# Kernel optimization log

Hardware: AMD Instinct MI355X
Metric: run time of the kernel (lower is better)

## Reference

```python
import jax, jax.numpy as jnp
import numpy as np

N_NODES = 50000
N_EDGES = 800000
IN_F, HID, HEADS, OUT_F = 64, 64, 4, 64
NEG_SLOPE = 0.2


def _gat_conv(x, ei, W, a_src, a_dst, b, H, C):
    """PyG-style GATConv (eval mode, add_self_loops=True, concat=True).
    x: [N, F_in], ei: [2, E], W: [F_in, H*C], a_src/a_dst: [H, C], b: [H*C].
    """
    N = x.shape[0]
    h = (x @ W).reshape(N, H, C)                      # [N,H,C]
    asrc = jnp.einsum('nhc,hc->nh', h, a_src)         # [N,H]
    adst = jnp.einsum('nhc,hc->nh', h, a_dst)         # [N,H]
    src, dst = ei[0], ei[1]
    logits = jax.nn.leaky_relu(asrc[src] + adst[dst], NEG_SLOPE)  # [E,H]
    m = jax.ops.segment_max(logits, dst, num_segments=N)
    m = jnp.where(jnp.isfinite(m), m, 0.0)
    ex = jnp.exp(logits - m[dst])
    denom = jax.ops.segment_sum(ex, dst, num_segments=N)
    alpha = ex / (denom[dst] + 1e-16)                 # [E,H]
    msg = h[src] * alpha[:, :, None]                  # [E,H,C]
    out = jax.ops.segment_sum(msg, dst, num_segments=N)  # [N,H,C]
    return out.reshape(N, H * C) + b


def _add_self_loops(ei, n):
    loops = jnp.arange(n, dtype=ei.dtype)
    return jnp.concatenate([ei, jnp.stack([loops, loops])], axis=1)


def setup_inputs() -> dict:
    key = jax.random.key(0)
    ks = jax.random.split(key, 16)
    x = jax.random.normal(ks[0], (N_NODES, IN_F), dtype=jnp.float32)
    edge_index = jax.random.randint(ks[1], (2, N_EDGES), 0, N_NODES, dtype=jnp.int32)
    s = 0.1
    d = {'x': x, 'edge_index': edge_index}
    # layer 0: IN_F -> HID, HEADS heads
    d['W0'] = jax.random.normal(ks[2], (IN_F, HEADS * HID), jnp.float32) * s
    d['a_src0'] = jax.random.normal(ks[3], (HEADS, HID), jnp.float32) * s
    d['a_dst0'] = jax.random.normal(ks[4], (HEADS, HID), jnp.float32) * s
    d['b0'] = jnp.zeros((HEADS * HID,), jnp.float32)
    # layer 1: HEADS*HID -> HID, HEADS heads
    d['W1'] = jax.random.normal(ks[5], (HEADS * HID, HEADS * HID), jnp.float32) * s
    d['a_src1'] = jax.random.normal(ks[6], (HEADS, HID), jnp.float32) * s
    d['a_dst1'] = jax.random.normal(ks[7], (HEADS, HID), jnp.float32) * s
    d['b1'] = jnp.zeros((HEADS * HID,), jnp.float32)
    # layer 2: HEADS*HID -> OUT_F, 1 head
    d['W2'] = jax.random.normal(ks[8], (HEADS * HID, OUT_F), jnp.float32) * s
    d['a_src2'] = jax.random.normal(ks[9], (1, OUT_F), jnp.float32) * s
    d['a_dst2'] = jax.random.normal(ks[10], (1, OUT_F), jnp.float32) * s
    d['b2'] = jnp.zeros((OUT_F,), jnp.float32)
    return d


def reference(x, edge_index, W0, a_src0, a_dst0, b0, W1, a_src1, a_dst1, b1, W2, a_src2, a_dst2, b2):
    ei = _add_self_loops(edge_index, x.shape[0])
    h = _gat_conv(x, ei, W0, a_src0, a_dst0, b0, HEADS, HID)
    h = jax.nn.elu(h)  # dropout identity in eval
    h = _gat_conv(h, ei, W1, a_src1, a_dst1, b1, HEADS, HID)
    h = jax.nn.elu(h)
    out = _gat_conv(h, ei, W2, a_src2, a_dst2, b2, 1, OUT_F)
    return out
```

## Files before the change

### kernel.cpp

```cpp
#include <hip/hip_runtime.h>
#include <hip/hip_fp16.h>
#include <math.h>

#define NODES 50000
#define EDGES 800000
#define NB_SCAN ((NODES + 1023) / 1024)

typedef __attribute__((ext_vector_type(8))) _Float16 f16x8;
typedef __attribute__((ext_vector_type(4))) _Float16 f16x4;
typedef __attribute__((ext_vector_type(4))) float f32x4;

__device__ __forceinline__ float lrelu02(float x){ return x > 0.f ? x : 0.2f * x; }

__device__ __forceinline__ f32x4 shflx4(f32x4 v, int m){
  f32x4 r;
  r[0] = __shfl_xor(v[0], m); r[1] = __shfl_xor(v[1], m);
  r[2] = __shfl_xor(v[2], m); r[3] = __shfl_xor(v[3], m);
  return r;
}


__global__ __launch_bounds__(256) void gat_hist(const int* __restrict__ ei, int* __restrict__ cnt){
  int e = blockIdx.x * 256 + threadIdx.x;
  if (e < EDGES) atomicAdd(&cnt[ei[EDGES + e]], 1);
}

__global__ __launch_bounds__(256) void gat_blocksum(const int* __restrict__ cnt, int* __restrict__ bsums){
  __shared__ int sd[256];
  int t = threadIdx.x, b = blockIdx.x;
  int base = b * 1024 + t * 4, s = 0;
  #pragma unroll
  for (int j = 0; j < 4; j++){ int i = base + j; if (i < NODES) s += cnt[i]; }
  sd[t] = s; __syncthreads();
  for (int o = 128; o > 0; o >>= 1){ if (t < o) sd[t] += sd[t + o]; __syncthreads(); }
  if (t == 0) bsums[b] = sd[0];
}

__global__ __launch_bounds__(256) void gat_rowptr(int* __restrict__ cnt, const int* __restrict__ bsums,
                                                  int* __restrict__ row_ptr){
  __shared__ int sd[256];
  int t = threadIdx.x, b = blockIdx.x;
  int base = b * 1024 + t * 4;
  int c[4]; int s = 0;
  #pragma unroll
  for (int j = 0; j < 4; j++){
    int i = base + j;
    c[j] = (i < NODES) ? cnt[i] : 0;
    s += c[j];
    if (i < NODES) cnt[i] = 0;
  }
  sd[t] = s; __syncthreads();
  for (int o = 1; o < 256; o <<= 1){
    int v = (t >= o) ? sd[t - o] : 0;
    __syncthreads();
    if (t >= o) sd[t] += v;
    __syncthreads();
  }
  int pre = 0;
  for (int i = 0; i < b; i++) pre += bsums[i];
  int off = pre + sd[t] - s;
  #pragma unroll
  for (int j = 0; j < 4; j++){
    int i = base + j;
    if (i < NODES){ row_ptr[i] = off; off += c[j]; }
  }
  if (b == 0 && t == 0) row_ptr[NODES] = EDGES;
}

__global__ __launch_bounds__(256) void gat_scatter(const int* __restrict__ ei, const int* __restrict__ row_ptr,
                                                    int* __restrict__ fill, int* __restrict__ col){
  int e = blockIdx.x * 256 + threadIdx.x;
  if (e < EDGES){
    int s = ei[e], d = ei[EDGES + e];
    int pos = row_ptr[d] + atomicAdd(&fill[d], 1);
    col[pos] = s;
  }
}


__global__ __launch_bounds__(256) void gat_prep(const float* __restrict__ x, _Float16* __restrict__ xh,
                                                const float* __restrict__ W0, const float* __restrict__ W1,
                                                const float* __restrict__ W2,
                                                _Float16* __restrict__ Wt0, _Float16* __restrict__ Wt1,
                                                _Float16* __restrict__ Wt2,
                                                const float* __restrict__ as0, const float* __restrict__ ad0,
                                                float* __restrict__ ws, float* __restrict__ wd,
                                                int* __restrict__ cnt){
  int b = blockIdx.x;
  int t = threadIdx.x;
  if (b < 3125){
    int i = b * 256 + t;
    float4 v = *(const float4*)(x + (size_t)i * 4);
    f16x4 h = { (_Float16)v.x, (_Float16)v.y, (_Float16)v.z, (_Float16)v.w };
    *(f16x4*)(xh + (size_t)i * 4) = h;
  } else if (b < 3701){
    int k = b - 3125;
    if (k < 64){
      Wt0[(size_t)t * 64 + k] = (_Float16)W0[(size_t)k * 256 + t];
    } else if (k < 320){
      int kk = k - 64;
      Wt1[(size_t)t * 256 + kk] = (_Float16)W1[(size_t)kk * 256 + t];
    } else {
      int kk = k - 320;
      if (t < 64) Wt2[(size_t)t * 256 + kk] = (_Float16)W2[(size_t)kk * 64 + t];
    }
  } else if (b == 3701){
    int h = t >> 6, c = t & 63;
    float s = 0.f, d = 0.f;
    for (int cc = 0; cc < 64; cc++){
      float w = W0[(size_t)c * 256 + h * 64 + cc];
      s += w * as0[h * 64 + cc];
      d += w * ad0[h * 64 + cc];
    }
    ws[h * 64 + c] = s;
    wd[h * 64 + c] = d;
  } else {
    int i = (b - 3702) * 256 + t;
    if (i < NODES) cnt[i] = 0;
  }
}


template<int K, int N, int ATTN>
__global__ __launch_bounds__(256) void gat_gemm_mfma(const _Float16* __restrict__ A, const _Float16* __restrict__ Wt,
                                                      _Float16* __restrict__ C,
                                                      const float* __restrict__ a_srcv, const float* __restrict__ a_dstv,
                                                      float* __restrict__ asrc, float* __restrict__ adst, int M){
  constexpr int NT = N / 64;
  constexpr int LDT = 72;
  __shared__ _Float16 As[64][LDT];
  __shared__ _Float16 Bs[N][LDT];

  int tid = threadIdx.x;
  int w = tid >> 6, l = tid & 63;
  int lg = l >> 4, lr = l & 15;
  int bm = blockIdx.x * 64;

  f32x4 acc[4][NT];
  #pragma unroll
  for (int m = 0; m < 4; m++)
    #pragma unroll
    for (int n = 0; n < NT; n++)
      acc[m][n] = (f32x4){0.f, 0.f, 0.f, 0.f};

  int ar = tid >> 2;
  int akc = (tid & 3) * 8;
  bool avalid = (bm + ar) < M;
  const _Float16* aptr = A + (size_t)(bm + ar) * K + akc;

  for (int k0 = 0; k0 < K; k0 += 64){
    float4 av0 = avalid ? *(const float4*)(aptr + k0)      : make_float4(0.f, 0.f, 0.f, 0.f);
    float4 av1 = avalid ? *(const float4*)(aptr + k0 + 32) : make_float4(0.f, 0.f, 0.f, 0.f);
    __syncthreads();
    *(float4*)&As[ar][akc]      = av0;
    *(float4*)&As[ar][akc + 32] = av1;
    #pragma unroll
    for (int c = 0; c < N / 32; c++){
      int idx = c * 256 + tid;
      int n = idx >> 3, kc = (idx & 7) * 8;
      *(float4*)&Bs[n][kc] = *(const float4*)(Wt + (size_t)n * K + k0 + kc);
    }
    __syncthreads();

    #pragma unroll
    for (int kk = 0; kk < 64; kk += 32){
      f16x8 af[4], bf[NT];
      #pragma unroll
      for (int m = 0; m < 4; m++) af[m] = *(const f16x8*)&As[16 * m + lr][kk + 8 * lg];
      #pragma unroll
      for (int n = 0; n < NT; n++) bf[n] = *(const f16x8*)&Bs[w * (N / 4) + 16 * n + lr][kk + 8 * lg];
      #pragma unroll
      for (int m = 0; m < 4; m++)
        #pragma unroll
        for (int n = 0; n < NT; n++)
          acc[m][n] = __builtin_amdgcn_mfma_f32_16x16x32_f16(af[m], bf[n], acc[m][n], 0, 0, 0);
    }
  }

  #pragma unroll
  for (int m = 0; m < 4; m++){
    #pragma unroll
    for (int j = 0; j < 4; j++){
      int row = bm + 16 * m + 4 * lg + j;
      if (row < M){
        #pragma unroll
        for (int n = 0; n < NT; n++)
          C[(size_t)row * N + w * (N / 4) + 16 * n + lr] = (_Float16)acc[m][n][j];
      }
    }
  }

  if constexpr (ATTN == 4){
    float avs[4], avd[4];
    #pragma unroll
    for (int n = 0; n < 4; n++){
      avs[n] = a_srcv[w * 64 + 16 * n + lr];
      avd[n] = a_dstv[w * 64 + 16 * n + lr];
    }
    #pragma unroll
    for (int m = 0; m < 4; m++){
      #pragma unroll
      for (int j = 0; j < 4; j++){
        float s1 = acc[m][0][j] * avs[0] + acc[m][1][j] * avs[1] + acc[m][2][j] * avs[2] + acc[m][3][j] * avs[3];
        float s2 = acc[m][0][j] * avd[0] + acc[m][1][j] * avd[1] + acc[m][2][j] * avd[2] + acc[m][3][j] * avd[3];
        #pragma unroll
        for (int o = 8; o > 0; o >>= 1){ s1 += __shfl_xor(s1, o); s2 += __shfl_xor(s2, o); }
        int row = bm + 16 * m + 4 * lg + j;
        if (lr == 0 && row < M){
          asrc[row * 4 + w] = s1;
          adst[row * 4 + w] = s2;
        }
      }
    }
  }
  if constexpr (ATTN == 1){
    __shared__ float sred[2][4][64];
    float av = a_srcv[w * 16 + lr], dv = a_dstv[w * 16 + lr];
    #pragma unroll
    for (int m = 0; m < 4; m++){
      #pragma unroll
      for (int j = 0; j < 4; j++){
        float s1 = acc[m][0][j] * av;
        float s2 = acc[m][0][j] * dv;
        #pragma unroll
        for (int o = 8; o > 0; o >>= 1){ s1 += __shfl_xor(s1, o); s2 += __shfl_xor(s2, o); }
        if (lr == 0){
          sred[0][w][16 * m + 4 * lg + j] = s1;
          sred[1][w][16 * m + 4 * lg + j] = s2;
        }
      }
    }
    __syncthreads();
    if (tid < 64){
      int row = bm + tid;
      if (row < M){
        asrc[row] = sred[0][0][tid] + sred[0][1][tid] + sred[0][2][tid] + sred[0][3][tid];
        adst[row] = sred[1][0][tid] + sred[1][1][tid] + sred[1][2][tid] + sred[1][3][tid];
      }
    }
  }
}


__global__ __launch_bounds__(256) void gat_gemm_bd(const _Float16* __restrict__ A, const _Float16* __restrict__ Bt,
                                                    const float* __restrict__ bias, _Float16* __restrict__ C, int M){
  int tid = threadIdx.x;
  int w = tid >> 6, l = tid & 63;
  int lg = l >> 4, lr = l & 15;
  int bm = blockIdx.x * 64;

  f32x4 acc[4][4];
  #pragma unroll
  for (int m = 0; m < 4; m++)
    #pragma unroll
    for (int n = 0; n < 4; n++)
      acc[m][n] = (f32x4){0.f, 0.f, 0.f, 0.f};

  f16x8 zf = {};
  #pragma unroll
  for (int ks = 0; ks < 2; ks++){
    int koff = ks * 32;
    f16x8 af[4], bf[4];
    #pragma unroll
    for (int m = 0; m < 4; m++){
      int row = bm + 16 * m + lr;
      af[m] = (row < M) ? *(const f16x8*)(A + (size_t)row * 256 + w * 64 + koff + 8 * lg) : zf;
    }
    #pragma unroll
    for (int n = 0; n < 4; n++)
      bf[n] = *(const f16x8*)(Bt + (size_t)(w * 64 + 16 * n + lr) * 64 + koff + 8 * lg);
    #pragma unroll
    for (int m = 0; m < 4; m++)
      #pragma unroll
      for (int n = 0; n < 4; n++)
        acc[m][n] = __builtin_amdgcn_mfma_f32_16x16x32_f16(af[m], bf[n], acc[m][n], 0, 0, 0);
  }

  #pragma unroll
  for (int m = 0; m < 4; m++){
    #pragma unroll
    for (int j = 0; j < 4; j++){
      int row = bm + 16 * m + 4 * lg + j;
      if (row < M){
        #pragma unroll
        for (int n = 0; n < 4; n++){
          int cc = w * 64 + 16 * n + lr;
          float o = acc[m][n][j] + bias[cc];
          o = o > 0.f ? o : expm1f(o);
          C[(size_t)row * 256 + cc] = (_Float16)o;
        }
      }
    }
  }
}


__global__ __launch_bounds__(256) void gat_attn0(const _Float16* __restrict__ xh, const float* __restrict__ ws,
                                                  const float* __restrict__ wd,
                                                  float* __restrict__ asrc, float* __restrict__ adst, int N){
  int lane = threadIdx.x & 63;
  int wid = threadIdx.x >> 6;
  int n = blockIdx.x * 4 + wid;
  if (n >= N) return;
  float v = (float)xh[(size_t)n * 64 + lane];
  #pragma unroll
  for (int h = 0; h < 4; h++){
    float s1 = v * ws[h * 64 + lane];
    float s2 = v * wd[h * 64 + lane];
    #pragma unroll
    for (int o = 32; o > 0; o >>= 1){ s1 += __shfl_xor(s1, o); s2 += __shfl_xor(s2, o); }
    if (lane == 0){ asrc[n * 4 + h] = s1; adst[n * 4 + h] = s2; }
  }
}


__global__ __launch_bounds__(256) void gat_edge_exp0n(const float* __restrict__ asrc, const float* __restrict__ adst,
                                                       const int* __restrict__ row_ptr, const int* __restrict__ col,
                                                       float* __restrict__ exf){
  int g = (blockIdx.x * 256 + threadIdx.x) >> 4;
  if (g >= NODES) return;
  int gl = threadIdx.x & 15;
  float4 b = *(const float4*)&adst[g * 4];
  int e0 = row_ptr[g], e1 = row_ptr[g + 1];
  for (int e = e0 + gl; e < e1; e += 16){
    int s = col[e];
    float4 a = *(const float4*)&asrc[s * 4];
    float4 r;
    r.x = __expf(lrelu02(a.x + b.x));
    r.y = __expf(lrelu02(a.y + b.y));
    r.z = __expf(lrelu02(a.z + b.z));
    r.w = __expf(lrelu02(a.w + b.w));
    *(float4*)&exf[(size_t)e * 4] = r;
  }
}


__global__ __launch_bounds__(256) void gat_aggregate_in64(const _Float16* __restrict__ xh, const float* __restrict__ exf,
                                                           const float* __restrict__ asrc, const float* __restrict__ adst,
                                                           const int* __restrict__ row_ptr, const int* __restrict__ col,
                                                           _Float16* __restrict__ agg){
  int lane = threadIdx.x & 63;
  int wid = threadIdx.x >> 6;
  int d = blockIdx.x * 4 + wid;
  if (d >= NODES) return;
  int slot = lane >> 4;
  int cpos = (lane & 15) * 4;

  f32x4 acc0 = {0,0,0,0}, acc1 = {0,0,0,0}, acc2 = {0,0,0,0}, acc3 = {0,0,0,0};
  f32x4 den = {0,0,0,0};

  int e0 = row_ptr[d], e1 = row_ptr[d + 1];
  const _Float16* xb = xh + cpos;
  int e = e0;
  for (; e + 8 <= e1; e += 8){
    int eA = e + slot, eB = e + 4 + slot;
    int sA = col[eA], sB = col[eB];
    float4 fA = *(const float4*)(exf + (size_t)eA * 4);
    float4 fB = *(const float4*)(exf + (size_t)eB * 4);
    f16x4 hA = *(const f16x4*)(xb + (size_t)sA * 64);
    f16x4 hB = *(const f16x4*)(xb + (size_t)sB * 64);
    f32x4 vA = { (float)hA[0], (float)hA[1], (float)hA[2], (float)hA[3] };
    f32x4 vB = { (float)hB[0], (float)hB[1], (float)hB[2], (float)hB[3] };
    den += (f32x4){ fA.x + fB.x, fA.y + fB.y, fA.z + fB.z, fA.w + fB.w };
    acc0 += fA.x * vA + fB.x * vB;
    acc1 += fA.y * vA + fB.y * vB;
    acc2 += fA.z * vA + fB.z * vB;
    acc3 += fA.w * vA + fB.w * vB;
  }
  if (e + 4 <= e1){
    int eA = e + slot;
    int sA = col[eA];
    float4 fA = *(const float4*)(exf + (size_t)eA * 4);
    f16x4 hA = *(const f16x4*)(xb + (size_t)sA * 64);
    f32x4 vA = { (float)hA[0], (float)hA[1], (float)hA[2], (float)hA[3] };
    den += (f32x4){ fA.x, fA.y, fA.z, fA.w };
    acc0 += fA.x * vA; acc1 += fA.y * vA; acc2 += fA.z * vA; acc3 += fA.w * vA;
    e += 4;
  }
  {
    int eA = e + slot;
    if (eA < e1){
      int sA = col[eA];
      float4 fA = *(const float4*)(exf + (size_t)eA * 4);
      f16x4 hA = *(const f16x4*)(xb + (size_t)sA * 64);
      f32x4 vA = { (float)hA[0], (float)hA[1], (float)hA[2], (float)hA[3] };
      den += (f32x4){ fA.x, fA.y, fA.z, fA.w };
      acc0 += fA.x * vA; acc1 += fA.y * vA; acc2 += fA.z * vA; acc3 += fA.w * vA;
    }
  }

  #pragma unroll
  for (int off = 16; off <= 32; off <<= 1){
    acc0 += shflx4(acc0, off);
    acc1 += shflx4(acc1, off);
    acc2 += shflx4(acc2, off);
    acc3 += shflx4(acc3, off);
    den  += shflx4(den,  off);
  }

  float4 a4 = *(const float4*)&asrc[d * 4];
  float4 b4 = *(const float4*)&adst[d * 4];
  float es0 = __expf(lrelu02(a4.x + b4.x));
  float es1 = __expf(lrelu02(a4.y + b4.y));
  float es2 = __expf(lrelu02(a4.z + b4.z));
  float es3 = __expf(lrelu02(a4.w + b4.w));
  f16x4 hs = *(const f16x4*)(xh + (size_t)d * 64 + cpos);
  f32x4 vs = { (float)hs[0], (float)hs[1], (float)hs[2], (float)hs[3] };
  acc0 += es0 * vs; acc1 += es1 * vs; acc2 += es2 * vs; acc3 += es3 * vs;
  den += (f32x4){ es0, es1, es2, es3 };

  if (slot == 0){
    float i0 = 1.f / (den[0] + 1e-16f), i1 = 1.f / (den[1] + 1e-16f);
    float i2 = 1.f / (den[2] + 1e-16f), i3 = 1.f / (den[3] + 1e-16f);
    _Float16* ob = agg + (size_t)d * 256 + cpos;
    f16x4 o0 = { (_Float16)(acc0[0]*i0), (_Float16)(acc0[1]*i0), (_Float16)(acc0[2]*i0), (_Float16)(acc0[3]*i0) };
    f16x4 o1 = { (_Float16)(acc1[0]*i1), (_Float16)(acc1[1]*i1), (_Float16)(acc1[2]*i1), (_Float16)(acc1[3]*i1) };
    f16x4 o2 = { (_Float16)(acc2[0]*i2), (_Float16)(acc2[1]*i2), (_Float16)(acc2[2]*i2), (_Float16)(acc2[3]*i2) };
    f16x4 o3 = { (_Float16)(acc3[0]*i3), (_Float16)(acc3[1]*i3), (_Float16)(acc3[2]*i3), (_Float16)(acc3[3]*i3) };
    *(f16x4*)(ob)       = o0;
    *(f16x4*)(ob + 64)  = o1;
    *(f16x4*)(ob + 128) = o2;
    *(f16x4*)(ob + 192) = o3;
  }
}


__global__ __launch_bounds__(256) void gat_aggregate4(const _Float16* __restrict__ hH, const float* __restrict__ asrc,
                                                       const float* __restrict__ adst,
                                                       const int* __restrict__ row_ptr, const int* __restrict__ col,
                                                       const float* __restrict__ bias, _Float16* __restrict__ out){
  int lane = threadIdx.x & 63;
  int wid = threadIdx.x >> 6;
  int d = blockIdx.x * 4 + wid;
  if (d >= NODES) return;
  int q = lane >> 4;
  int co = lane * 4;

  float adq = adst[d * 4 + q];

  float ex = __expf(lrelu02(asrc[d * 4 + q] + adq));
  f16x4 hv = *(const f16x4*)(hH + (size_t)d * 256 + co);
  float4 acc = make_float4(ex * (float)hv[0], ex * (float)hv[1], ex * (float)hv[2], ex * (float)hv[3]);
  float den = ex;

  int e0 = row_ptr[d], e1 = row_ptr[d + 1];
  const _Float16* hbase = hH + co;
  int e = e0;
  for (; e + 4 <= e1; e += 4){
    int s0 = col[e], s1 = col[e + 1], s2 = col[e + 2], s3 = col[e + 3];
    float a0 = asrc[s0 * 4 + q], a1 = asrc[s1 * 4 + q], a2 = asrc[s2 * 4 + q], a3 = asrc[s3 * 4 + q];
    f16x4 h0 = *(const f16x4*)(hbase + (size_t)s0 * 256);
    f16x4 h1 = *(const f16x4*)(hbase + (size_t)s1 * 256);
    f16x4 h2 = *(const f16x4*)(hbase + (size_t)s2 * 256);
    f16x4 h3 = *(const f16x4*)(hbase + (size_t)s3 * 256);
    float x0 = __expf(lrelu02(a0 + adq));
    float x1 = __expf(lrelu02(a1 + adq));
    float x2 = __expf(lrelu02(a2 + adq));
    float x3 = __expf(lrelu02(a3 + adq));
    den += x0 + x1 + x2 + x3;
    acc.x += x0 * (float)h0[0] + x1 * (float)h1[0] + x2 * (float)h2[0] + x3 * (float)h3[0];
    acc.y += x0 * (float)h0[1] + x1 * (float)h1[1] + x2 * (float)h2[1] + x3 * (float)h3[1];
    acc.z += x0 * (float)h0[2] + x1 * (float)h1[2] + x2 * (float)h2[2] + x3 * (float)h3[2];
    acc.w += x0 * (float)h0[3] + x1 * (float)h1[3] + x2 * (float)h2[3] + x3 * (float)h3[3];
  }
  for (; e < e1; e++){
    int s0 = col[e];
    float a0 = asrc[s0 * 4 + q];
    f16x4 h0 = *(const f16x4*)(hbase + (size_t)s0 * 256);
    float x0 = __expf(lrelu02(a0 + adq));
    den += x0;
    acc.x += x0 * (float)h0[0]; acc.y += x0 * (float)h0[1];
    acc.z += x0 * (float)h0[2]; acc.w += x0 * (float)h0[3];
  }

  float inv = 1.f / (den + 1e-16f);
  float4 b4 = *(const float4*)&bias[co];
  float4 o = make_float4(acc.x * inv + b4.x, acc.y * inv + b4.y, acc.z * inv + b4.z, acc.w * inv + b4.w);
  o.x = o.x > 0.f ? o.x : expm1f(o.x);
  o.y = o.y > 0.f ? o.y : expm1f(o.y);
  o.z = o.z > 0.f ? o.z : expm1f(o.z);
  o.w = o.w > 0.f ? o.w : expm1f(o.w);
  f16x4 oh = { (_Float16)o.x, (_Float16)o.y, (_Float16)o.z, (_Float16)o.w };
  *(f16x4*)(out + (size_t)d * 256 + co) = oh;
}


__global__ __launch_bounds__(256) void gat_aggregate1n(const _Float16* __restrict__ hH,
                                                        const float* __restrict__ asrc, const float* __restrict__ adst,
                                                        const int* __restrict__ row_ptr, const int* __restrict__ col,
                                                        const float* __restrict__ bias, float* __restrict__ out){
  int lane = threadIdx.x & 63;
  int wid = threadIdx.x >> 6;
  int d = blockIdx.x * 4 + wid;
  if (d >= NODES) return;
  int slot = lane >> 4;
  int cpos = (lane & 15) * 4;

  float adq = adst[d];
  f32x4 acc = {0,0,0,0};
  float den = 0.f;

  int e0 = row_ptr[d], e1 = row_ptr[d + 1];
  const _Float16* hb = hH + cpos;
  int e = e0;
  for (; e + 8 <= e1; e += 8){
    int eA = e + slot, eB = e + 4 + slot;
    int sA = col[eA], sB = col[eB];
    float fA = __expf(lrelu02(asrc[sA] + adq));
    float fB = __expf(lrelu02(asrc[sB] + adq));
    f16x4 hA = *(const f16x4*)(hb + (size_t)sA * 64);
    f16x4 hB = *(const f16x4*)(hb + (size_t)sB * 64);
    f32x4 vA = { (float)hA[0], (float)hA[1], (float)hA[2], (float)hA[3] };
    f32x4 vB = { (float)hB[0], (float)hB[1], (float)hB[2], (float)hB[3] };
    den += fA + fB;
    acc += fA * vA + fB * vB;
  }
  if (e + 4 <= e1){
    int eA = e + slot;
    int sA = col[eA];
    float fA = __expf(lrelu02(asrc[sA] + adq));
    f16x4 hA = *(const f16x4*)(hb + (size_t)sA * 64);
    f32x4 vA = { (float)hA[0], (float)hA[1], (float)hA[2], (float)hA[3] };
    den += fA; acc += fA * vA;
    e += 4;
  }
  {
    int eA = e + slot;
    if (eA < e1){
      int sA = col[eA];
      float fA = __expf(lrelu02(asrc[sA] + adq));
      f16x4 hA = *(const f16x4*)(hb + (size_t)sA * 64);
      f32x4 vA = { (float)hA[0], (float)hA[1], (float)hA[2], (float)hA[3] };
      den += fA; acc += fA * vA;
    }
  }

  #pragma unroll
  for (int off = 16; off <= 32; off <<= 1){
    acc += shflx4(acc, off);
    den += __shfl_xor(den, off);
  }

  float es = __expf(lrelu02(asrc[d] + adq));
  f16x4 hs = *(const f16x4*)(hH + (size_t)d * 64 + cpos);
  f32x4 vs = { (float)hs[0], (float)hs[1], (float)hs[2], (float)hs[3] };
  acc += es * vs;
  den += es;

  if (slot == 0){
    float inv = 1.f / (den + 1e-16f);
    float4 b4 = *(const float4*)&bias[cpos];
    float4 o = make_float4(acc[0] * inv + b4.x, acc[1] * inv + b4.y, acc[2] * inv + b4.z, acc[3] * inv + b4.w);
    *(float4*)(out + (size_t)d * 64 + cpos) = o;
  }
}


extern "C" void kernel_launch(void* const* d_in, const int* in_sizes, int n_in,
                              void* d_out, int out_size, void* d_ws, size_t ws_size,
                              hipStream_t stream) {
  const float* x   = (const float*)d_in[0];
  const int*   ei  = (const int*)  d_in[1];
  const float* W0  = (const float*)d_in[2];
  const float* as0 = (const float*)d_in[3];
  const float* ad0 = (const float*)d_in[4];
  const float* b0  = (const float*)d_in[5];
  const float* W1  = (const float*)d_in[6];
  const float* as1 = (const float*)d_in[7];
  const float* ad1 = (const float*)d_in[8];
  const float* b1  = (const float*)d_in[9];
  const float* W2  = (const float*)d_in[10];
  const float* as2 = (const float*)d_in[11];
  const float* ad2 = (const float*)d_in[12];
  const float* b2  = (const float*)d_in[13];
  float* out = (float*)d_out;

  auto al = [](size_t v){ return (v + 255) & ~(size_t)255; };
  char* p = (char*)d_ws;
  int*      row_ptr = (int*)p;      p += al((NODES + 1) * sizeof(int));
  int*      cnt     = (int*)p;      p += al(NODES * sizeof(int));
  int*      bsums   = (int*)p;      p += al(64 * sizeof(int));
  int*      col     = (int*)p;      p += al(EDGES * sizeof(int));
  float*    exf     = (float*)p;    p += al((size_t)EDGES * 4 * sizeof(float));
  float*    asrc    = (float*)p;    p += al(NODES * 4 * sizeof(float));
  float*    adst    = (float*)p;    p += al(NODES * 4 * sizeof(float));
  _Float16* xh      = (_Float16*)p; p += al((size_t)NODES * 64 * sizeof(_Float16));
  _Float16* hH      = (_Float16*)p; p += al((size_t)NODES * 256 * sizeof(_Float16));
  _Float16* actb    = (_Float16*)p; p += al((size_t)NODES * 256 * sizeof(_Float16));
  _Float16* Wt0     = (_Float16*)p; p += al(256 * 64 * sizeof(_Float16));
  _Float16* Wt1     = (_Float16*)p; p += al(256 * 256 * sizeof(_Float16));
  _Float16* Wt2     = (_Float16*)p; p += al(64 * 256 * sizeof(_Float16));
  float*    ws0     = (float*)p;    p += al(256 * sizeof(float));
  float*    wd0     = (float*)p;    p += al(256 * sizeof(float));

  gat_prep<<<3898, 256, 0, stream>>>(x, xh, W0, W1, W2, Wt0, Wt1, Wt2, as0, ad0, ws0, wd0, cnt);

  gat_hist<<<(EDGES + 255) / 256, 256, 0, stream>>>(ei, cnt);
  gat_blocksum<<<NB_SCAN, 256, 0, stream>>>(cnt, bsums);
  gat_rowptr<<<NB_SCAN, 256, 0, stream>>>(cnt, bsums, row_ptr);
  gat_scatter<<<(EDGES + 255) / 256, 256, 0, stream>>>(ei, row_ptr, cnt, col);

  const int nodeBlocks = (NODES + 3) / 4;
  const int gemmBlocks = (NODES + 63) / 64;
  const int expBlocks  = (NODES * 16 + 255) / 256;

  gat_attn0<<<nodeBlocks, 256, 0, stream>>>(xh, ws0, wd0, asrc, adst, NODES);
  gat_edge_exp0n<<<expBlocks, 256, 0, stream>>>(asrc, adst, row_ptr, col, exf);
  gat_aggregate_in64<<<nodeBlocks, 256, 0, stream>>>(xh, exf, asrc, adst, row_ptr, col, hH);
  gat_gemm_bd<<<gemmBlocks, 256, 0, stream>>>(hH, Wt0, b0, actb, NODES);

  gat_gemm_mfma<256, 256, 4><<<gemmBlocks, 256, 0, stream>>>(actb, Wt1, hH, as1, ad1, asrc, adst, NODES);
  gat_aggregate4<<<nodeBlocks, 256, 0, stream>>>(hH, asrc, adst, row_ptr, col, b1, actb);

  gat_gemm_mfma<256, 64, 1><<<gemmBlocks, 256, 0, stream>>>(actb, Wt2, hH, as2, ad2, asrc, adst, NODES);
  gat_aggregate1n<<<nodeBlocks, 256, 0, stream>>>(hH, asrc, adst, row_ptr, col, b2, out);
}
```

Measured before the change: 332.3 us.

## Fuse layer-0 head-diagonal GEMM with ELU into layer-1 GEMM via LDS

```diff
diff --git a/kernel.cpp b/kernel.cpp
--- a/kernel.cpp
+++ b/kernel.cpp
@@ -121,11 +121,135 @@
 }
 
 
-template<int K, int N, int ATTN>
-__global__ __launch_bounds__(256) void gat_gemm_mfma(const _Float16* __restrict__ A, const _Float16* __restrict__ Wt,
-                                                      _Float16* __restrict__ C,
+__global__ __launch_bounds__(256) void gat_gemm_l0l1(const _Float16* __restrict__ agg, const _Float16* __restrict__ Bt0,
+                                                      const float* __restrict__ bias0,
+                                                      const _Float16* __restrict__ Wt1, _Float16* __restrict__ C,
                                                       const float* __restrict__ a_srcv, const float* __restrict__ a_dstv,
                                                       float* __restrict__ asrc, float* __restrict__ adst, int M){
+  __shared__ _Float16 Asf[64][264];
+  __shared__ _Float16 Bs[256][40];
+
+  int tid = threadIdx.x;
+  int w = tid >> 6, l = tid & 63;
+  int lg = l >> 4, lr = l & 15;
+  int bm = blockIdx.x * 64;
+
+  {
+    f32x4 acc1[4][4];
+    #pragma unroll
+    for (int m = 0; m < 4; m++)
+      #pragma unroll
+      for (int n = 0; n < 4; n++)
+        acc1[m][n] = (f32x4){0.f, 0.f, 0.f, 0.f};
+
+    f16x8 zf = {};
+    #pragma unroll
+    for (int ks = 0; ks < 2; ks++){
+      int koff = ks * 32;
+      f16x8 af[4], bf[4];
+      #pragma unroll
+      for (int m = 0; m < 4; m++){
+        int row = bm + 16 * m + lr;
+        af[m] = (row < M) ? *(const f16x8*)(agg + (size_t)row * 256 + w * 64 + koff + 8 * lg) : zf;
+      }
+      #pragma unroll
+      for (int n = 0; n < 4; n++)
+        bf[n] = *(const f16x8*)(Bt0 + (size_t)(w * 64 + 16 * n + lr) * 64 + koff + 8 * lg);
+      #pragma unroll
+      for (int m = 0; m < 4; m++)
+        #pragma unroll
+        for (int n = 0; n < 4; n++)
+          acc1[m][n] = __builtin_amdgcn_mfma_f32_16x16x32_f16(af[m], bf[n], acc1[m][n], 0, 0, 0);
+    }
+
+    #pragma unroll
+    for (int m = 0; m < 4; m++){
+      #pragma unroll
+      for (int j = 0; j < 4; j++){
+        int r16 = 16 * m + 4 * lg + j;
+        bool valid = (bm + r16) < M;
+        #pragma unroll
+        for (int n = 0; n < 4; n++){
+          int cc = w * 64 + 16 * n + lr;
+          float o = acc1[m][n][j] + bias0[cc];
+          o = o > 0.f ? o : expm1f(o);
+          Asf[r16][cc] = valid ? (_Float16)o : (_Float16)0.f;
+        }
+      }
+    }
+  }
+
+  f32x4 acc[4][4];
+  #pragma unroll
+  for (int m = 0; m < 4; m++)
+    #pragma unroll
+    for (int n = 0; n < 4; n++)
+      acc[m][n] = (f32x4){0.f, 0.f, 0.f, 0.f};
+
+  for (int k0 = 0; k0 < 256; k0 += 32){
+    __syncthreads();
+    #pragma unroll
+    for (int c = 0; c < 4; c++){
+      int idx = c * 256 + tid;
+      int n = idx >> 2, kc = (idx & 3) * 8;
+      *(float4*)&Bs[n][kc] = *(const float4*)(Wt1 + (size_t)n * 256 + k0 + kc);
+    }
+    __syncthreads();
+
+    f16x8 af[4], bf[4];
+    #pragma unroll
+    for (int m = 0; m < 4; m++) af[m] = *(const f16x8*)&Asf[16 * m + lr][k0 + 8 * lg];
+    #pragma unroll
+    for (int n = 0; n < 4; n++) bf[n] = *(const f16x8*)&Bs[w * 64 + 16 * n + lr][8 * lg];
+    #pragma unroll
+    for (int m = 0; m < 4; m++)
+      #pragma unroll
+      for (int n = 0; n < 4; n++)
+        acc[m][n] = __builtin_amdgcn_mfma_f32_16x16x32_f16(af[m], bf[n], acc[m][n], 0, 0, 0);
+  }
+
+  #pragma unroll
+  for (int m = 0; m < 4; m++){
+    #pragma unroll
+    for (int j = 0; j < 4; j++){
+      int row = bm + 16 * m + 4 * lg + j;
+      if (row < M){
+        #pragma unroll
+        for (int n = 0; n < 4; n++)
+          C[(size_t)row * 256 + w * 64 + 16 * n + lr] = (_Float16)acc[m][n][j];
+      }
+    }
+  }
+
+  float avs[4], avd[4];
+  #pragma unroll
+  for (int n = 0; n < 4; n++){
+    avs[n] = a_srcv[w * 64 + 16 * n + lr];
+    avd[n] = a_dstv[w * 64 + 16 * n + lr];
+  }
+  #pragma unroll
+  for (int m = 0; m < 4; m++){
+    #pragma unroll
+    for (int j = 0; j < 4; j++){
+      float s1 = acc[m][0][j] * avs[0] + acc[m][1][j] * avs[1] + acc[m][2][j] * avs[2] + acc[m][3][j] * avs[3];
+      float s2 = acc[m][0][j] * avd[0] + acc[m][1][j] * avd[1] + acc[m][2][j] * avd[2] + acc[m][3][j] * avd[3];
+      #pragma unroll
+      for (int o = 8; o > 0; o >>= 1){ s1 += __shfl_xor(s1, o); s2 += __shfl_xor(s2, o); }
+      int row = bm + 16 * m + 4 * lg + j;
+      if (lr == 0 && row < M){
+        asrc[row * 4 + w] = s1;
+        adst[row * 4 + w] = s2;
+      }
+    }
+  }
+}
+
+
+template<int K, int N>
+__global__ __launch_bounds__(256) void gat_gemm_mfma1(const _Float16* __restrict__ A, const _Float16* __restrict__ Wt,
+                                                       _Float16* __restrict__ C,
+                                                       const float* __restrict__ a_srcv, const float* __restrict__ a_dstv,
+                                                       float* __restrict__ asrc, float* __restrict__ adst, int M){
   constexpr int NT = N / 64;
   constexpr int LDT = 72;
   __shared__ _Float16 As[64][LDT];
@@ -190,106 +314,28 @@
     }
   }
 
-  if constexpr (ATTN == 4){
-    float avs[4], avd[4];
-    #pragma unroll
-    for (int n = 0; n < 4; n++){
-      avs[n] = a_srcv[w * 64 + 16 * n + lr];
-      avd[n] = a_dstv[w * 64 + 16 * n + lr];
-    }
-    #pragma unroll
-    for (int m = 0; m < 4; m++){
-      #pragma unroll
-      for (int j = 0; j < 4; j++){
-        float s1 = acc[m][0][j] * avs[0] + acc[m][1][j] * avs[1] + acc[m][2][j] * avs[2] + acc[m][3][j] * avs[3];
-        float s2 = acc[m][0][j] * avd[0] + acc[m][1][j] * avd[1] + acc[m][2][j] * avd[2] + acc[m][3][j] * avd[3];
-        #pragma unroll
-        for (int o = 8; o > 0; o >>= 1){ s1 += __shfl_xor(s1, o); s2 += __shfl_xor(s2, o); }
-        int row = bm + 16 * m + 4 * lg + j;
-        if (lr == 0 && row < M){
-          asrc[row * 4 + w] = s1;
-          adst[row * 4 + w] = s2;
-        }
+  __shared__ float sred[2][4][64];
+  float av = a_srcv[w * 16 + lr], dv = a_dstv[w * 16 + lr];
+  #pragma unroll
+  for (int m = 0; m < 4; m++){
+    #pragma unroll
+    for (int j = 0; j < 4; j++){
+      float s1 = acc[m][0][j] * av;
+      float s2 = acc[m][0][j] * dv;
+      #pragma unroll
+      for (int o = 8; o > 0; o >>= 1){ s1 += __shfl_xor(s1, o); s2 += __shfl_xor(s2, o); }
+      if (lr == 0){
+        sred[0][w][16 * m + 4 * lg + j] = s1;
+        sred[1][w][16 * m + 4 * lg + j] = s2;
       }
     }
   }
-  if constexpr (ATTN == 1){
-    __shared__ float sred[2][4][64];
-    float av = a_srcv[w * 16 + lr], dv = a_dstv[w * 16 + lr];
-    #pragma unroll
-    for (int m = 0; m < 4; m++){
-      #pragma unroll
-      for (int j = 0; j < 4; j++){
-        float s1 = acc[m][0][j] * av;
-        float s2 = acc[m][0][j] * dv;
-        #pragma unroll
-        for (int o = 8; o > 0; o >>= 1){ s1 += __shfl_xor(s1, o); s2 += __shfl_xor(s2, o); }
-        if (lr == 0){
-          sred[0][w][16 * m + 4 * lg + j] = s1;
-          sred[1][w][16 * m + 4 * lg + j] = s2;
-        }
-      }
-    }
-    __syncthreads();
-    if (tid < 64){
-      int row = bm + tid;
-      if (row < M){
-        asrc[row] = sred[0][0][tid] + sred[0][1][tid] + sred[0][2][tid] + sred[0][3][tid];
-        adst[row] = sred[1][0][tid] + sred[1][1][tid] + sred[1][2][tid] + sred[1][3][tid];
-      }
-    }
-  }
-}
-
-
-__global__ __launch_bounds__(256) void gat_gemm_bd(const _Float16* __restrict__ A, const _Float16* __restrict__ Bt,
-                                                    const float* __restrict__ bias, _Float16* __restrict__ C, int M){
-  int tid = threadIdx.x;
-  int w = tid >> 6, l = tid & 63;
-  int lg = l >> 4, lr = l & 15;
-  int bm = blockIdx.x * 64;
-
-  f32x4 acc[4][4];
-  #pragma unroll
-  for (int m = 0; m < 4; m++)
-    #pragma unroll
-    for (int n = 0; n < 4; n++)
-      acc[m][n] = (f32x4){0.f, 0.f, 0.f, 0.f};
-
-  f16x8 zf = {};
-  #pragma unroll
-  for (int ks = 0; ks < 2; ks++){
-    int koff = ks * 32;
-    f16x8 af[4], bf[4];
-    #pragma unroll
-    for (int m = 0; m < 4; m++){
-      int row = bm + 16 * m + lr;
-      af[m] = (row < M) ? *(const f16x8*)(A + (size_t)row * 256 + w * 64 + koff + 8 * lg) : zf;
-    }
-    #pragma unroll
-    for (int n = 0; n < 4; n++)
-      bf[n] = *(const f16x8*)(Bt + (size_t)(w * 64 + 16 * n + lr) * 64 + koff + 8 * lg);
-    #pragma unroll
-    for (int m = 0; m < 4; m++)
-      #pragma unroll
-      for (int n = 0; n < 4; n++)
-        acc[m][n] = __builtin_amdgcn_mfma_f32_16x16x32_f16(af[m], bf[n], acc[m][n], 0, 0, 0);
-  }
-
-  #pragma unroll
-  for (int m = 0; m < 4; m++){
-    #pragma unroll
-    for (int j = 0; j < 4; j++){
-      int row = bm + 16 * m + 4 * lg + j;
-      if (row < M){
-        #pragma unroll
-        for (int n = 0; n < 4; n++){
-          int cc = w * 64 + 16 * n + lr;
-          float o = acc[m][n][j] + bias[cc];
-          o = o > 0.f ? o : expm1f(o);
-          C[(size_t)row * 256 + cc] = (_Float16)o;
-        }
-      }
+  __syncthreads();
+  if (tid < 64){
+    int row = bm + tid;
+    if (row < M){
+      asrc[row] = sred[0][0][tid] + sred[0][1][tid] + sred[0][2][tid] + sred[0][3][tid];
+      adst[row] = sred[1][0][tid] + sred[1][1][tid] + sred[1][2][tid] + sred[1][3][tid];
     }
   }
 }
@@ -607,11 +653,11 @@
   gat_attn0<<<nodeBlocks, 256, 0, stream>>>(xh, ws0, wd0, asrc, adst, NODES);
   gat_edge_exp0n<<<expBlocks, 256, 0, stream>>>(asrc, adst, row_ptr, col, exf);
   gat_aggregate_in64<<<nodeBlocks, 256, 0, stream>>>(xh, exf, asrc, adst, row_ptr, col, hH);
-  gat_gemm_bd<<<gemmBlocks, 256, 0, stream>>>(hH, Wt0, b0, actb, NODES);
-
-  gat_gemm_mfma<256, 256, 4><<<gemmBlocks, 256, 0, stream>>>(actb, Wt1, hH, as1, ad1, asrc, adst, NODES);
-  gat_aggregate4<<<nodeBlocks, 256, 0, stream>>>(hH, asrc, adst, row_ptr, col, b1, actb);
-
-  gat_gemm_mfma<256, 64, 1><<<gemmBlocks, 256, 0, stream>>>(actb, Wt2, hH, as2, ad2, asrc, adst, NODES);
-  gat_aggregate1n<<<nodeBlocks, 256, 0, stream>>>(hH, asrc, adst, row_ptr, col, b2, out);
-}
+
+  gat_gemm_l0l1<<<gemmBlocks, 256, 0, stream>>>(hH, Wt0, b0, Wt1, actb, as1, ad1, asrc, adst, NODES);
+
+  gat_aggregate4<<<nodeBlocks, 256, 0, stream>>>(actb, asrc, adst, row_ptr, col, b1, hH);
+
+  gat_gemm_mfma1<256, 64><<<gemmBlocks, 256, 0, stream>>>(hH, Wt2, actb, as2, ad2, asrc, adst, NODES);
+  gat_aggregate1n<<<nodeBlocks, 256, 0, stream>>>(actb, asrc, adst, row_ptr, col, b2, out);
+}
```

New measurement: 314.6 us. -5.4%, faster.
